# Performance work log

Hardware: AMD Instinct MI355X
Metric: run time of the kernel (lower is better)

## Reference

```python
import jax, jax.numpy as jnp
import numpy as np

N_SRC = 100000
N_DST = 50000
N_EDGES = 800000
D = 64
D_OUT = 64
ALPHA = 0.1


def setup_inputs() -> dict:
    key = jax.random.key(0)
    ks = jax.random.split(key, 6)
    H_src = jax.random.normal(ks[0], (N_SRC, D), dtype=jnp.float32)
    H_dst = jax.random.normal(ks[1], (N_DST, D), dtype=jnp.float32)
    HBar = jax.random.normal(ks[2], (N_DST, D), dtype=jnp.float32)
    src_idx = jax.random.randint(ks[3], (N_EDGES,), 0, N_SRC, dtype=jnp.int32)
    dst_idx = jnp.sort(jax.random.randint(ks[4], (N_EDGES,), 0, N_DST, dtype=jnp.int32))
    # Xavier-uniform-ish linear params (gain folded into scale)
    W = jax.random.normal(ks[5], (D_OUT, 2 * D), dtype=jnp.float32) * (1.0 / np.sqrt(2 * D))
    b = jnp.zeros((D_OUT,), dtype=jnp.float32)
    return {"H_src": H_src, "H_dst": H_dst, "HBar": HBar,
            "src_idx": src_idx, "dst_idx": dst_idx, "W": W, "b": b}


def reference(H_src, H_dst, HBar, src_idx, dst_idx, W, b):
    # update_all(copy_u, mean): per-dst mean of incoming src features
    msgs = H_src[src_idx]                                   # [E, D]
    sums = jax.ops.segment_sum(msgs, dst_idx, num_segments=N_DST)   # [N_DST, D]
    cnt = jax.ops.segment_sum(jnp.ones((N_EDGES,), jnp.float32), dst_idx,
                              num_segments=N_DST)           # [N_DST]
    HDelta_new = sums / jnp.maximum(cnt, 1.0)[:, None]      # mean; 0 for deg-0 nodes
    # control-variate blend: alpha-weighted detached correction
    h_neigh = (1.0 - ALPHA) * jax.lax.stop_gradient(HBar - HDelta_new) + HDelta_new
    # linear on concat([H_dst, h_neigh]) + relu (dropout=0 => identity)
    h = jnp.concatenate([H_dst, h_neigh], axis=1) @ W.T + b  # [N_DST, D_OUT]
    h = jax.nn.relu(h)
    return h, h_neigh
```

## Files before the change

### kernel.cpp

```cpp
#include <hip/hip_runtime.h>

#define N_SRC_C   100000
#define N_DST_C   50000
#define N_EDGES_C 800000
#define D_C       64
#define ONE_MINUS_ALPHA 0.9f
#define ALPHA_C        0.1f

#define CONV_ITEMS (N_SRC_C * D_C / 4)
#define PREP_BLOCKS ((CONV_ITEMS + 255) / 256)

typedef __attribute__((ext_vector_type(8))) short bf16x8;
typedef __attribute__((ext_vector_type(4))) float f32x4;

__device__ __forceinline__ ushort f32_to_bf16(float f) {
    uint u = __float_as_uint(f);
    return (ushort)((u + 0x7fffu + ((u >> 16) & 1u)) >> 16);
}

__global__ __launch_bounds__(256) void prep_kernel(
    const float* __restrict__ H_src, ushort* __restrict__ Hb,
    const int* __restrict__ dst_idx, int* __restrict__ row_ptr,
    const float* __restrict__ W, ushort* __restrict__ WB)
{
    const int t = blockIdx.x * 256 + threadIdx.x;

    if (t < CONV_ITEMS) {
        const float4 v = reinterpret_cast<const float4*>(H_src)[t];
        ushort4 o;
        o.x = f32_to_bf16(v.x); o.y = f32_to_bf16(v.y);
        o.z = f32_to_bf16(v.z); o.w = f32_to_bf16(v.w);
        reinterpret_cast<ushort4*>(Hb)[t] = o;
    }

    if (t < N_EDGES_C) {
        const int d = dst_idx[t];
        const int p = (t == 0) ? -1 : dst_idx[t - 1];
        for (int n = p + 1; n <= d; ++n) row_ptr[n] = t;
        if (t == N_EDGES_C - 1) {
            for (int n = d + 1; n <= N_DST_C; ++n) row_ptr[n] = N_EDGES_C;
        }
    }

    if (t < 4 * 4 * 64 * 8) {
        const int j    = t & 7;
        const int lane = (t >> 3) & 63;
        const int ks   = (t >> 9) & 3;
        const int ob   = t >> 11;
        const int o = ob * 16 + (lane & 15);
        const int k = ks * 32 + ((lane >> 4) << 3) + j;
        WB[t] = f32_to_bf16(W[o * 128 + k]);
    }
}

__global__ __launch_bounds__(256) void sage_fused_kernel(
    const ushort* __restrict__ Hb,
    const float*  __restrict__ H_dst,
    const float*  __restrict__ HBar,
    const int*    __restrict__ src_idx,
    const int*    __restrict__ row_ptr,
    const ushort* __restrict__ WB,
    const float*  __restrict__ b,
    float*        __restrict__ h_out,
    float*        __restrict__ hn_out)
{
    __shared__ __align__(16) ushort Xs[32][136];

    const int lane = threadIdx.x & 63;
    const int w    = threadIdx.x >> 6;
    const int g    = lane >> 3;
    const int c    = lane & 7;
    const int base = blockIdx.x * 32;
    const int r    = w * 8 + g;
    int node = base + r;
    if (node > N_DST_C - 1) node = N_DST_C - 1;

    const int s0 = row_ptr[node];
    const int s1 = row_ptr[node + 1];

    float acc[8];
    #pragma unroll
    for (int i = 0; i < 8; ++i) acc[i] = 0.f;

    int idxA = 0, idxB = 0;
    if (s0 < s1) {
        int pA = s0 + c;     if (pA >= s1) pA = s1 - 1;
        int pB = s0 + 8 + c; if (pB >= s1) pB = s1 - 1;
        idxA = src_idx[pA];
        idxB = src_idx[pB];
    }

    for (int e = s0; e < s1; e += 16) {
        int nA = 0, nB = 0;
        if (e + 16 < s1) {
            int pA = e + 16 + c; if (pA >= s1) pA = s1 - 1;
            int pB = e + 24 + c; if (pB >= s1) pB = s1 - 1;
            nA = src_idx[pA];
            nB = src_idx[pB];
        }
        #pragma unroll
        for (int j = 0; j < 8; ++j) {
            const int ij = __shfl(idxA, g * 8 + j);
            if (e + j < s1) {
                const uint4 p = *reinterpret_cast<const uint4*>(
                    Hb + (size_t)ij * D_C + c * 8);
                acc[0] += __uint_as_float(p.x << 16);
                acc[1] += __uint_as_float(p.x & 0xffff0000u);
                acc[2] += __uint_as_float(p.y << 16);
                acc[3] += __uint_as_float(p.y & 0xffff0000u);
                acc[4] += __uint_as_float(p.z << 16);
                acc[5] += __uint_as_float(p.z & 0xffff0000u);
                acc[6] += __uint_as_float(p.w << 16);
                acc[7] += __uint_as_float(p.w & 0xffff0000u);
            }
        }
        #pragma unroll
        for (int j = 0; j < 8; ++j) {
            const int ij = __shfl(idxB, g * 8 + j);
            if (e + 8 + j < s1) {
                const uint4 p = *reinterpret_cast<const uint4*>(
                    Hb + (size_t)ij * D_C + c * 8);
                acc[0] += __uint_as_float(p.x << 16);
                acc[1] += __uint_as_float(p.x & 0xffff0000u);
                acc[2] += __uint_as_float(p.y << 16);
                acc[3] += __uint_as_float(p.y & 0xffff0000u);
                acc[4] += __uint_as_float(p.z << 16);
                acc[5] += __uint_as_float(p.z & 0xffff0000u);
                acc[6] += __uint_as_float(p.w << 16);
                acc[7] += __uint_as_float(p.w & 0xffff0000u);
            }
        }
        idxA = nA; idxB = nB;
    }

    const int cnt = s1 - s0;
    const float inv = (cnt > 0) ? (ALPHA_C / (float)cnt) : 0.0f;

    const size_t hbase = (size_t)node * D_C + c * 8;
    const float4 hb0 = *reinterpret_cast<const float4*>(HBar + hbase);
    const float4 hb1 = *reinterpret_cast<const float4*>(HBar + hbase + 4);
    float o[8];
    o[0] = ONE_MINUS_ALPHA * hb0.x + acc[0] * inv;
    o[1] = ONE_MINUS_ALPHA * hb0.y + acc[1] * inv;
    o[2] = ONE_MINUS_ALPHA * hb0.z + acc[2] * inv;
    o[3] = ONE_MINUS_ALPHA * hb0.w + acc[3] * inv;
    o[4] = ONE_MINUS_ALPHA * hb1.x + acc[4] * inv;
    o[5] = ONE_MINUS_ALPHA * hb1.y + acc[5] * inv;
    o[6] = ONE_MINUS_ALPHA * hb1.z + acc[6] * inv;
    o[7] = ONE_MINUS_ALPHA * hb1.w + acc[7] * inv;

    *reinterpret_cast<float4*>(hn_out + hbase)     = make_float4(o[0], o[1], o[2], o[3]);
    *reinterpret_cast<float4*>(hn_out + hbase + 4) = make_float4(o[4], o[5], o[6], o[7]);

    union { ushort u[8]; bf16x8 v; } hi, lo;
    #pragma unroll
    for (int i = 0; i < 8; ++i) hi.u[i] = f32_to_bf16(o[i]);
    *reinterpret_cast<bf16x8*>(&Xs[r][64 + c * 8]) = hi.v;

    const float4 d0 = *reinterpret_cast<const float4*>(H_dst + hbase);
    const float4 d1 = *reinterpret_cast<const float4*>(H_dst + hbase + 4);
    lo.u[0] = f32_to_bf16(d0.x); lo.u[1] = f32_to_bf16(d0.y);
    lo.u[2] = f32_to_bf16(d0.z); lo.u[3] = f32_to_bf16(d0.w);
    lo.u[4] = f32_to_bf16(d1.x); lo.u[5] = f32_to_bf16(d1.y);
    lo.u[6] = f32_to_bf16(d1.z); lo.u[7] = f32_to_bf16(d1.w);
    *reinterpret_cast<bf16x8*>(&Xs[r][c * 8]) = lo.v;

    __syncthreads();

    const int tile  = w >> 1;
    const int ob0   = (w & 1) * 2;
    const int row16 = lane & 15;
    const int kg    = lane >> 4;

    bf16x8 af[4];
    #pragma unroll
    for (int ks = 0; ks < 4; ++ks)
        af[ks] = *reinterpret_cast<const bf16x8*>(&Xs[tile * 16 + row16][kg * 8 + ks * 32]);

    #pragma unroll
    for (int oi = 0; oi < 2; ++oi) {
        const int ob = ob0 + oi;
        f32x4 cacc = {0.f, 0.f, 0.f, 0.f};
        #pragma unroll
        for (int ks = 0; ks < 4; ++ks) {
            const bf16x8 bf = *reinterpret_cast<const bf16x8*>(
                WB + ((size_t)(ob * 4 + ks) * 64 + lane) * 8);
            cacc = __builtin_amdgcn_mfma_f32_16x16x32_bf16(af[ks], bf, cacc, 0, 0, 0);
        }
        const float bias = b[ob * 16 + row16];
        #pragma unroll
        for (int rr = 0; rr < 4; ++rr) {
            int gn = base + tile * 16 + kg * 4 + rr;
            if (gn > N_DST_C - 1) gn = N_DST_C - 1;
            h_out[(size_t)gn * D_C + ob * 16 + row16] = fmaxf(cacc[rr] + bias, 0.0f);
        }
    }
}

extern "C" void kernel_launch(void* const* d_in, const int* in_sizes, int n_in,
                              void* d_out, int out_size, void* d_ws, size_t ws_size,
                              hipStream_t stream) {
    const float* H_src   = (const float*)d_in[0];
    const float* H_dst   = (const float*)d_in[1];
    const float* HBar    = (const float*)d_in[2];
    const int*   src_idx = (const int*)d_in[3];
    const int*   dst_idx = (const int*)d_in[4];
    const float* W       = (const float*)d_in[5];
    const float* b       = (const float*)d_in[6];

    float* out    = (float*)d_out;
    float* h_out  = out;
    float* hn_out = out + (size_t)N_DST_C * D_C;

    int*    row_ptr = (int*)d_ws;
    ushort* WB      = (ushort*)((char*)d_ws + (256 << 10));
    ushort* Hb      = (ushort*)((char*)d_ws + (512 << 10));

    hipLaunchKernelGGL(prep_kernel, dim3(PREP_BLOCKS), dim3(256), 0, stream,
                       H_src, Hb, dst_idx, row_ptr, W, WB);

    hipLaunchKernelGGL(sage_fused_kernel, dim3((N_DST_C + 31) / 32), dim3(256), 0, stream,
                       Hb, H_dst, HBar, src_idx, row_ptr, WB, b, h_out, hn_out);
}
```

Measured before the change: 36.92 us.

## Store gathered source features as FP8 and process 64 nodes per block

Source features are packed into FP8 (e4m3) instead of bf16 in the prep kernel, which halves the bytes each gathered edge row costs. Each row is now read by 4 lanes of 16 bytes instead of 8 lanes. The fused kernel is restructured so each block handles 64 destination nodes, 16 per wave, and each wave computes all four output blocks of the MFMA linear layer. The FP8 encode and decode is done in software and loses precision in the neighbour mean, which could break tolerance. It also adds ALU work per gathered element.

Measured after the change: 40.08 us. 1.09x slower.

```diff
diff --git a/kernel.cpp b/kernel.cpp
--- a/kernel.cpp
+++ b/kernel.cpp
@@ -18,8 +18,33 @@
     return (ushort)((u + 0x7fffu + ((u >> 16) & 1u)) >> 16);
 }
 
+__device__ __forceinline__ uint f32_to_fp8(float x) {
+    const uint u = __float_as_uint(x);
+    const uint s = (u >> 24) & 0x80u;
+    const float af = fabsf(x);
+    if (af < 0.015625f) {
+        const uint m = (uint)(int)rintf(af * 512.0f);
+        return s | m;
+    }
+    if (af >= 448.0f) return s | 0x7Eu;
+    const uint a = u & 0x7fffffffu;
+    const uint r = a + 0x7FFFFu + ((a >> 20) & 1u);
+    const uint e8 = (r >> 23) - 120u;
+    const uint m8 = (r >> 20) & 7u;
+    return s | (e8 << 3) | m8;
+}
+
+__device__ __forceinline__ void acc_fp8x4(uint v, float* acc) {
+    #pragma unroll
+    for (int k = 0; k < 4; ++k) {
+        const uint t = v << (24 - 8 * k);
+        const uint f = (t & 0x80000000u) | ((t >> 4) & 0x07F00000u);
+        acc[k] = fmaf(__uint_as_float(f), 0x1p120f, acc[k]);
+    }
+}
+
 __global__ __launch_bounds__(256) void prep_kernel(
-    const float* __restrict__ H_src, ushort* __restrict__ Hb,
+    const float* __restrict__ H_src, uint* __restrict__ Hf8,
     const int* __restrict__ dst_idx, int* __restrict__ row_ptr,
     const float* __restrict__ W, ushort* __restrict__ WB)
 {
@@ -27,10 +52,8 @@
 
     if (t < CONV_ITEMS) {
         const float4 v = reinterpret_cast<const float4*>(H_src)[t];
-        ushort4 o;
-        o.x = f32_to_bf16(v.x); o.y = f32_to_bf16(v.y);
-        o.z = f32_to_bf16(v.z); o.w = f32_to_bf16(v.w);
-        reinterpret_cast<ushort4*>(Hb)[t] = o;
+        Hf8[t] = f32_to_fp8(v.x) | (f32_to_fp8(v.y) << 8) |
+                 (f32_to_fp8(v.z) << 16) | (f32_to_fp8(v.w) << 24);
     }
 
     if (t < N_EDGES_C) {
@@ -54,7 +77,7 @@
 }
 
 __global__ __launch_bounds__(256) void sage_fused_kernel(
-    const ushort* __restrict__ Hb,
+    const uchar*  __restrict__ Hf8,
     const float*  __restrict__ H_dst,
     const float*  __restrict__ HBar,
     const int*    __restrict__ src_idx,
@@ -64,122 +87,109 @@
     float*        __restrict__ h_out,
     float*        __restrict__ hn_out)
 {
-    __shared__ __align__(16) ushort Xs[32][136];
+    __shared__ __align__(16) ushort Xs[64][136];
 
     const int lane = threadIdx.x & 63;
     const int w    = threadIdx.x >> 6;
-    const int g    = lane >> 3;
-    const int c    = lane & 7;
-    const int base = blockIdx.x * 32;
-    const int r    = w * 8 + g;
+    const int g    = lane >> 2;
+    const int c    = lane & 3;
+    const int base = blockIdx.x * 64;
+    const int r    = w * 16 + g;
     int node = base + r;
     if (node > N_DST_C - 1) node = N_DST_C - 1;
 
     const int s0 = row_ptr[node];
     const int s1 = row_ptr[node + 1];
 
-    float acc[8];
-    #pragma unroll
-    for (int i = 0; i < 8; ++i) acc[i] = 0.f;
-
-    int idxA = 0, idxB = 0;
+    float acc[16];
+    #pragma unroll
+    for (int i = 0; i < 16; ++i) acc[i] = 0.f;
+
+    int idxA[4];
+    #pragma unroll
+    for (int k = 0; k < 4; ++k) idxA[k] = 0;
     if (s0 < s1) {
-        int pA = s0 + c;     if (pA >= s1) pA = s1 - 1;
-        int pB = s0 + 8 + c; if (pB >= s1) pB = s1 - 1;
-        idxA = src_idx[pA];
-        idxB = src_idx[pB];
+        #pragma unroll
+        for (int k = 0; k < 4; ++k) {
+            int p = s0 + 4 * c + k; if (p >= s1) p = s1 - 1;
+            idxA[k] = src_idx[p];
+        }
     }
 
     for (int e = s0; e < s1; e += 16) {
-        int nA = 0, nB = 0;
+        int idxN[4];
+        #pragma unroll
+        for (int k = 0; k < 4; ++k) idxN[k] = 0;
         if (e + 16 < s1) {
-            int pA = e + 16 + c; if (pA >= s1) pA = s1 - 1;
-            int pB = e + 24 + c; if (pB >= s1) pB = s1 - 1;
-            nA = src_idx[pA];
-            nB = src_idx[pB];
-        }
-        #pragma unroll
-        for (int j = 0; j < 8; ++j) {
-            const int ij = __shfl(idxA, g * 8 + j);
+            #pragma unroll
+            for (int k = 0; k < 4; ++k) {
+                int p = e + 16 + 4 * c + k; if (p >= s1) p = s1 - 1;
+                idxN[k] = src_idx[p];
+            }
+        }
+        #pragma unroll
+        for (int j = 0; j < 16; ++j) {
+            const int ij = __shfl(idxA[j & 3], (lane & 0x3C) | (j >> 2));
             if (e + j < s1) {
                 const uint4 p = *reinterpret_cast<const uint4*>(
-                    Hb + (size_t)ij * D_C + c * 8);
-                acc[0] += __uint_as_float(p.x << 16);
-                acc[1] += __uint_as_float(p.x & 0xffff0000u);
-                acc[2] += __uint_as_float(p.y << 16);
-                acc[3] += __uint_as_float(p.y & 0xffff0000u);
-                acc[4] += __uint_as_float(p.z << 16);
-                acc[5] += __uint_as_float(p.z & 0xffff0000u);
-                acc[6] += __uint_as_float(p.w << 16);
-                acc[7] += __uint_as_float(p.w & 0xffff0000u);
+                    Hf8 + (size_t)ij * 64 + c * 16);
+                acc_fp8x4(p.x, acc + 0);
+                acc_fp8x4(p.y, acc + 4);
+                acc_fp8x4(p.z, acc + 8);
+                acc_fp8x4(p.w, acc + 12);
             }
         }
-        #pragma unroll
-        for (int j = 0; j < 8; ++j) {
-            const int ij = __shfl(idxB, g * 8 + j);
-            if (e + 8 + j < s1) {
-                const uint4 p = *reinterpret_cast<const uint4*>(
-                    Hb + (size_t)ij * D_C + c * 8);
-                acc[0] += __uint_as_float(p.x << 16);
-                acc[1] += __uint_as_float(p.x & 0xffff0000u);
-                acc[2] += __uint_as_float(p.y << 16);
-                acc[3] += __uint_as_float(p.y & 0xffff0000u);
-                acc[4] += __uint_as_float(p.z << 16);
-                acc[5] += __uint_as_float(p.z & 0xffff0000u);
-                acc[6] += __uint_as_float(p.w << 16);
-                acc[7] += __uint_as_float(p.w & 0xffff0000u);
-            }
-        }
-        idxA = nA; idxB = nB;
+        idxA[0] = idxN[0]; idxA[1] = idxN[1];
+        idxA[2] = idxN[2]; idxA[3] = idxN[3];
     }
 
     const int cnt = s1 - s0;
     const float inv = (cnt > 0) ? (ALPHA_C / (float)cnt) : 0.0f;
 
-    const size_t hbase = (size_t)node * D_C + c * 8;
-    const float4 hb0 = *reinterpret_cast<const float4*>(HBar + hbase);
-    const float4 hb1 = *reinterpret_cast<const float4*>(HBar + hbase + 4);
-    float o[8];
-    o[0] = ONE_MINUS_ALPHA * hb0.x + acc[0] * inv;
-    o[1] = ONE_MINUS_ALPHA * hb0.y + acc[1] * inv;
-    o[2] = ONE_MINUS_ALPHA * hb0.z + acc[2] * inv;
-    o[3] = ONE_MINUS_ALPHA * hb0.w + acc[3] * inv;
-    o[4] = ONE_MINUS_ALPHA * hb1.x + acc[4] * inv;
-    o[5] = ONE_MINUS_ALPHA * hb1.y + acc[5] * inv;
-    o[6] = ONE_MINUS_ALPHA * hb1.z + acc[6] * inv;
-    o[7] = ONE_MINUS_ALPHA * hb1.w + acc[7] * inv;
-
-    *reinterpret_cast<float4*>(hn_out + hbase)     = make_float4(o[0], o[1], o[2], o[3]);
-    *reinterpret_cast<float4*>(hn_out + hbase + 4) = make_float4(o[4], o[5], o[6], o[7]);
-
-    union { ushort u[8]; bf16x8 v; } hi, lo;
-    #pragma unroll
-    for (int i = 0; i < 8; ++i) hi.u[i] = f32_to_bf16(o[i]);
-    *reinterpret_cast<bf16x8*>(&Xs[r][64 + c * 8]) = hi.v;
-
-    const float4 d0 = *reinterpret_cast<const float4*>(H_dst + hbase);
-    const float4 d1 = *reinterpret_cast<const float4*>(H_dst + hbase + 4);
-    lo.u[0] = f32_to_bf16(d0.x); lo.u[1] = f32_to_bf16(d0.y);
-    lo.u[2] = f32_to_bf16(d0.z); lo.u[3] = f32_to_bf16(d0.w);
-    lo.u[4] = f32_to_bf16(d1.x); lo.u[5] = f32_to_bf16(d1.y);
-    lo.u[6] = f32_to_bf16(d1.z); lo.u[7] = f32_to_bf16(d1.w);
-    *reinterpret_cast<bf16x8*>(&Xs[r][c * 8]) = lo.v;
+    const size_t hbase = (size_t)node * D_C + c * 16;
+    float o[16];
+    #pragma unroll
+    for (int t4 = 0; t4 < 4; ++t4) {
+        const float4 hb = *reinterpret_cast<const float4*>(HBar + hbase + t4 * 4);
+        o[t4 * 4 + 0] = ONE_MINUS_ALPHA * hb.x + acc[t4 * 4 + 0] * inv;
+        o[t4 * 4 + 1] = ONE_MINUS_ALPHA * hb.y + acc[t4 * 4 + 1] * inv;
+        o[t4 * 4 + 2] = ONE_MINUS_ALPHA * hb.z + acc[t4 * 4 + 2] * inv;
+        o[t4 * 4 + 3] = ONE_MINUS_ALPHA * hb.w + acc[t4 * 4 + 3] * inv;
+        *reinterpret_cast<float4*>(hn_out + hbase + t4 * 4) =
+            make_float4(o[t4 * 4 + 0], o[t4 * 4 + 1], o[t4 * 4 + 2], o[t4 * 4 + 3]);
+    }
+
+    union { ushort u[8]; bf16x8 v; } pk;
+    #pragma unroll
+    for (int i = 0; i < 8; ++i) pk.u[i] = f32_to_bf16(o[i]);
+    *reinterpret_cast<bf16x8*>(&Xs[r][64 + c * 16]) = pk.v;
+    #pragma unroll
+    for (int i = 0; i < 8; ++i) pk.u[i] = f32_to_bf16(o[8 + i]);
+    *reinterpret_cast<bf16x8*>(&Xs[r][64 + c * 16 + 8]) = pk.v;
+
+    #pragma unroll
+    for (int half = 0; half < 2; ++half) {
+        const float4 d0 = *reinterpret_cast<const float4*>(H_dst + hbase + half * 8);
+        const float4 d1 = *reinterpret_cast<const float4*>(H_dst + hbase + half * 8 + 4);
+        pk.u[0] = f32_to_bf16(d0.x); pk.u[1] = f32_to_bf16(d0.y);
+        pk.u[2] = f32_to_bf16(d0.z); pk.u[3] = f32_to_bf16(d0.w);
+        pk.u[4] = f32_to_bf16(d1.x); pk.u[5] = f32_to_bf16(d1.y);
+        pk.u[6] = f32_to_bf16(d1.z); pk.u[7] = f32_to_bf16(d1.w);
+        *reinterpret_cast<bf16x8*>(&Xs[r][c * 16 + half * 8]) = pk.v;
+    }
 
     __syncthreads();
 
-    const int tile  = w >> 1;
-    const int ob0   = (w & 1) * 2;
     const int row16 = lane & 15;
     const int kg    = lane >> 4;
 
     bf16x8 af[4];
     #pragma unroll
     for (int ks = 0; ks < 4; ++ks)
-        af[ks] = *reinterpret_cast<const bf16x8*>(&Xs[tile * 16 + row16][kg * 8 + ks * 32]);
-
-    #pragma unroll
-    for (int oi = 0; oi < 2; ++oi) {
-        const int ob = ob0 + oi;
+        af[ks] = *reinterpret_cast<const bf16x8*>(&Xs[w * 16 + row16][kg * 8 + ks * 32]);
+
+    #pragma unroll
+    for (int ob = 0; ob < 4; ++ob) {
         f32x4 cacc = {0.f, 0.f, 0.f, 0.f};
         #pragma unroll
         for (int ks = 0; ks < 4; ++ks) {
@@ -190,7 +200,7 @@
         const float bias = b[ob * 16 + row16];
         #pragma unroll
         for (int rr = 0; rr < 4; ++rr) {
-            int gn = base + tile * 16 + kg * 4 + rr;
+            int gn = base + w * 16 + kg * 4 + rr;
             if (gn > N_DST_C - 1) gn = N_DST_C - 1;
             h_out[(size_t)gn * D_C + ob * 16 + row16] = fmaxf(cacc[rr] + bias, 0.0f);
         }
@@ -214,11 +224,12 @@
 
     int*    row_ptr = (int*)d_ws;
     ushort* WB      = (ushort*)((char*)d_ws + (256 << 10));
-    ushort* Hb      = (ushort*)((char*)d_ws + (512 << 10));
+    uint*   Hf8     = (uint*)((char*)d_ws + (512 << 10));
 
     hipLaunchKernelGGL(prep_kernel, dim3(PREP_BLOCKS), dim3(256), 0, stream,
-                       H_src, Hb, dst_idx, row_ptr, W, WB);
-
-    hipLaunchKernelGGL(sage_fused_kernel, dim3((N_DST_C + 31) / 32), dim3(256), 0, stream,
-                       Hb, H_dst, HBar, src_idx, row_ptr, WB, b, h_out, hn_out);
-}
+                       H_src, Hf8, dst_idx, row_ptr, W, WB);
+
+    hipLaunchKernelGGL(sage_fused_kernel, dim3((N_DST_C + 63) / 64), dim3(256), 0, stream,
+                       (const uchar*)Hf8, H_dst, HBar, src_idx, row_ptr, WB, b,
+                       h_out, hn_out);
+}
```
